# Kernel optimization log

Measured on AMD Instinct MI355X. Metric: run time of the kernel, lower is better.

Reference implementation:

```python
import jax, jax.numpy as jnp
import numpy as np

L1, L2, B, D1, D2, HEADS, M = 1024, 1024, 8, 512, 1024, 16, 1024
DPH = M // HEADS  # 64


def setup_inputs() -> dict:
    key = jax.random.key(0)
    ks = jax.random.split(key, 10)
    w = lambda k, shp: jax.random.normal(k, shp, jnp.float32) * 0.02
    z = lambda n: jnp.zeros((n,), jnp.float32)
    return {
        "ctx_1": jax.random.normal(ks[0], (L1, B, D1), jnp.float32),
        "ctx_2": jax.random.normal(ks[1], (L2, B, D2), jnp.float32),
        "Wk1": w(ks[2], (M, D1)), "bk1": z(M),
        "Wv1": w(ks[3], (M, D1)), "bv1": z(M),
        "Wk2": w(ks[4], (M, D2)), "bk2": z(M),
        "Wv2": w(ks[5], (M, D2)), "bv2": z(M),
        "Wf12": w(ks[6], (M, M)), "bf12": z(M),
        "Wf21": w(ks[7], (M, M)), "bf21": z(M),
    }


def _shape_heads(x):
    # [L, B, M] -> [B, H, L, dph]
    L, Bs, _ = x.shape
    return x.reshape(L, Bs, HEADS, DPH).transpose(1, 2, 0, 3)


def _unshape(x):
    # [B, H, L, dph] -> [L, B, M]
    Bs, Hn, L, d = x.shape
    return x.transpose(2, 0, 1, 3).reshape(L, Bs, Hn * d)


def reference(ctx_1, ctx_2, Wk1, bk1, Wv1, bv1, Wk2, bk2, Wv2, bv2,
              Wf12, bf12, Wf21, bf21):
    k1 = _shape_heads(ctx_1 @ Wk1.T + bk1)  # [B,H,L1,d]
    v1 = _shape_heads(ctx_1 @ Wv1.T + bv1)  # [B,H,L1,d]
    k2 = _shape_heads(ctx_2 @ Wk2.T + bk2)  # [B,H,L2,d]
    v2 = _shape_heads(ctx_2 @ Wv2.T + bv2)  # [B,H,L2,d]

    # scores: key_2 @ key_1^T -> [B, H, L2, L1]
    scores = jnp.einsum('bhqd,bhkd->bhqk', k2, k1)

    # direction 1 -> 2: softmax over dim=2 (the L2 axis), then AV with value_1
    dist_1_to_2 = jax.nn.softmax(scores, axis=2)
    context_1_to_2 = jnp.einsum('bhqk,bhkd->bhqd', dist_1_to_2, v1)  # [B,H,L2,d]
    context_1_to_2 = _unshape(context_1_to_2) @ Wf12.T + bf12        # [L2,B,M]

    # direction 2 -> 1: softmax over dim=1 (the head axis), transpose, AV with value_2
    dist_2_to_1 = jax.nn.softmax(scores, axis=1)
    context_2_to_1 = jnp.einsum('bhqk,bhqd->bhkd', dist_2_to_1, v2)  # [B,H,L1,d]
    context_2_to_1 = _unshape(context_2_to_1) @ Wf21.T + bf21        # [L1,B,M]

    return (context_2_to_1, context_1_to_2)
```

## Files before the change

### kernel.cpp

```cpp
#include <hip/hip_runtime.h>
#include <hip/hip_bf16.h>

constexpr int LQ  = 1024;
constexpr int BN  = 8;
constexpr int D1N = 512;
constexpr int D2N = 1024;
constexpr int HN  = 16;
constexpr int MN  = 1024;
constexpr int DPH = 64;

typedef __attribute__((ext_vector_type(8)))  short bf16x8;
typedef __attribute__((ext_vector_type(2)))  float f32x2;
typedef __attribute__((ext_vector_type(4)))  float f32x4;
typedef __attribute__((ext_vector_type(16))) float f32x16;

__device__ __forceinline__ unsigned short f2bf(float f) {
  unsigned u = __float_as_uint(f);
  u += 0x7FFFu + ((u >> 16) & 1u);
  return (unsigned short)(u >> 16);
}
__device__ __forceinline__ float bf2f(unsigned short u) {
  return __uint_as_float(((unsigned)u) << 16);
}
__device__ __forceinline__ float rcpf(float x) {
  float r;
  asm("v_rcp_f32 %0, %1" : "=v"(r) : "v"(x));
  return r;
}

__device__ __forceinline__ f32x4 mfma16(bf16x8 a, bf16x8 b, f32x4 c) {
  return __builtin_amdgcn_mfma_f32_16x16x32_bf16(a, b, c, 0, 0, 0);
}
__device__ __forceinline__ f32x16 mfma32(bf16x8 a, bf16x8 b, f32x16 c) {
  return __builtin_amdgcn_mfma_f32_32x32x16_bf16(a, b, c, 0, 0, 0);
}
__device__ __forceinline__ f32x16 zero16() {
  f32x16 z;
#pragma unroll
  for (int i = 0; i < 16; ++i) z[i] = 0.f;
  return z;
}

__device__ __forceinline__ unsigned cvtpk(float lo, float hi) {
  unsigned r;
  asm("v_cvt_pk_bf16_f32 %0, %1, %2" : "=v"(r) : "v"(lo), "v"(hi));
  return r;
}

__device__ __forceinline__ void lds_barrier() {
  asm volatile("s_waitcnt lgkmcnt(0)" ::: "memory");
  __builtin_amdgcn_s_barrier();
}

__device__ __forceinline__ bf16x8 pfrag(const float* p) {
  unsigned x0 = cvtpk(p[0], p[1]), y0 = cvtpk(p[4], p[5]);
  unsigned x1 = cvtpk(p[2], p[3]), y1 = cvtpk(p[6], p[7]);
  asm volatile("v_permlane32_swap_b32 %0, %1" : "+v"(x0), "+v"(y0));
  asm volatile("v_permlane32_swap_b32 %0, %1" : "+v"(x1), "+v"(y1));
  union { unsigned u[4]; bf16x8 v; } r;
  r.u[0] = x0; r.u[1] = x1; r.u[2] = y0; r.u[3] = y1;
  return r.v;
}

__device__ __forceinline__ bf16x8 pack8(f32x4 p0, f32x4 p1) {
  bf16x8 o;
  o[0] = (short)f2bf(p0[0]); o[1] = (short)f2bf(p0[1]);
  o[2] = (short)f2bf(p0[2]); o[3] = (short)f2bf(p0[3]);
  o[4] = (short)f2bf(p1[0]); o[5] = (short)f2bf(p1[1]);
  o[6] = (short)f2bf(p1[2]); o[7] = (short)f2bf(p1[3]);
  return o;
}
__device__ __forceinline__ bf16x8 pack8q(f32x4 lo, f32x4 hi) {
  union { unsigned u[4]; bf16x8 v; } r;
  r.u[0] = cvtpk(lo[0], lo[1]); r.u[1] = cvtpk(lo[2], lo[3]);
  r.u[2] = cvtpk(hi[0], hi[1]); r.u[3] = cvtpk(hi[2], hi[3]);
  return r.v;
}

__global__ __launch_bounds__(256) void cvt_kernel(const float* __restrict__ src,
                                                  unsigned short* __restrict__ dst,
                                                  int n8) {
  int i = blockIdx.x * blockDim.x + threadIdx.x;
  if (i >= n8) return;
  const f32x4* s = (const f32x4*)src;
  f32x4 x = s[2 * i], y = s[2 * i + 1];
  ((bf16x8*)dst)[i] = pack8(x, y);
}

template <int K, int MODE, bool AF32>
__device__ __forceinline__ void gemm_body(const void* __restrict__ Ap,
                                          const unsigned short* __restrict__ W,
                                          const float* __restrict__ bias,
                                          void* __restrict__ outp,
                                          int rowb, int colb) {
  __shared__ unsigned short As[128 * 40], Bs[128 * 40];
  const int tid = threadIdx.x, wave = tid >> 6, lane = tid & 63;
  const int lg = lane >> 4, lm = lane & 15;
  const int wrow = (wave >> 1) * 64, wcol = (wave & 1) * 64;
  const int sr = tid >> 1, sh = (tid & 1) * 16;
  const unsigned short* Arow = AF32 ? nullptr
      : (const unsigned short*)Ap + (size_t)(rowb + sr) * K + sh;
  const float* ArowF = AF32 ? (const float*)Ap + (size_t)(rowb + sr) * K + sh
                            : nullptr;
  const unsigned short* Wrow = W + (size_t)(colb + sr) * K + sh;

  f32x4 acc[4][4];
#pragma unroll
  for (int i = 0; i < 4; ++i)
#pragma unroll
    for (int j = 0; j < 4; ++j) acc[i][j] = (f32x4){0.f, 0.f, 0.f, 0.f};

  f32x4 fa0, fa1, fa2, fa3;
  bf16x8 a0, a1, b0, b1;
  if (AF32) {
    fa0 = *(const f32x4*)(ArowF);     fa1 = *(const f32x4*)(ArowF + 4);
    fa2 = *(const f32x4*)(ArowF + 8); fa3 = *(const f32x4*)(ArowF + 12);
  } else {
    a0 = *(const bf16x8*)(Arow);
    a1 = *(const bf16x8*)(Arow + 8);
  }
  b0 = *(const bf16x8*)(Wrow);
  b1 = *(const bf16x8*)(Wrow + 8);

  for (int kk = 0; kk < K; kk += 32) {
    lds_barrier();
    if (AF32) {
      *(bf16x8*)&As[sr * 40 + sh]     = pack8q(fa0, fa1);
      *(bf16x8*)&As[sr * 40 + sh + 8] = pack8q(fa2, fa3);
    } else {
      *(bf16x8*)&As[sr * 40 + sh] = a0;
      *(bf16x8*)&As[sr * 40 + sh + 8] = a1;
    }
    *(bf16x8*)&Bs[sr * 40 + sh] = b0;
    *(bf16x8*)&Bs[sr * 40 + sh + 8] = b1;
    const int kn = (kk + 32 < K) ? kk + 32 : 0;
    if (AF32) {
      fa0 = *(const f32x4*)(ArowF + kn);     fa1 = *(const f32x4*)(ArowF + kn + 4);
      fa2 = *(const f32x4*)(ArowF + kn + 8); fa3 = *(const f32x4*)(ArowF + kn + 12);
    } else {
      a0 = *(const bf16x8*)(Arow + kn);
      a1 = *(const bf16x8*)(Arow + kn + 8);
    }
    b0 = *(const bf16x8*)(Wrow + kn);
    b1 = *(const bf16x8*)(Wrow + kn + 8);
    lds_barrier();
    bf16x8 af[4], wf[4];
#pragma unroll
    for (int i = 0; i < 4; ++i) af[i] = *(const bf16x8*)&As[(wrow + i * 16 + lm) * 40 + lg * 8];
#pragma unroll
    for (int j = 0; j < 4; ++j) wf[j] = *(const bf16x8*)&Bs[(wcol + j * 16 + lm) * 40 + lg * 8];
#pragma unroll
    for (int i = 0; i < 4; ++i)
#pragma unroll
      for (int j = 0; j < 4; ++j) acc[i][j] = mfma16(af[i], wf[j], acc[i][j]);
  }

#pragma unroll
  for (int j = 0; j < 4; ++j) {
    int col = colb + wcol + j * 16 + lm;
    float bs = bias[col];
#pragma unroll
    for (int i = 0; i < 4; ++i) {
#pragma unroll
      for (int r = 0; r < 4; ++r) {
        int row = rowb + wrow + i * 16 + lg * 4 + r;
        float v = acc[i][j][r] + bs;
        if (MODE == 0) {
          int l = row >> 3, bb = row & 7, h = col >> 6, d = col & 63;
          ((unsigned short*)outp)[(((size_t)(bb * HN + h)) * LQ + l) * DPH + d] = f2bf(v);
        } else {
          ((float*)outp)[(size_t)row * MN + col] = v;
        }
      }
    }
  }
}

template <int K>
__global__ __launch_bounds__(256) void gemm_pair_f32_kernel(
    const float* __restrict__ A,
    const unsigned short* __restrict__ W0, const unsigned short* __restrict__ W1,
    const float* __restrict__ b0, const float* __restrict__ b1,
    void* __restrict__ o0, void* __restrict__ o1) {
  const int sel = blockIdx.x & 1;
  gemm_body<K, 0, true>(A, sel ? W1 : W0, sel ? b1 : b0, sel ? o1 : o0,
                        (blockIdx.x >> 1) * 128, blockIdx.y * 128);
}

template <int K>
__global__ __launch_bounds__(256) void gemm_dual_kernel(
    const unsigned short* __restrict__ A0, const unsigned short* __restrict__ A1,
    const unsigned short* __restrict__ W0, const unsigned short* __restrict__ W1,
    const float* __restrict__ b0, const float* __restrict__ b1,
    void* __restrict__ o0, void* __restrict__ o1) {
  const int sel = blockIdx.y >> 3;
  gemm_body<K, 2, false>(sel ? A1 : A0, sel ? W1 : W0, sel ? b1 : b0,
                         sel ? o1 : o0, blockIdx.x * 128, (blockIdx.y & 7) * 128);
}

__global__ __launch_bounds__(256) void transpose_kernel(const unsigned short* __restrict__ V,
                                                        unsigned short* __restrict__ VT,
                                                        const float* __restrict__ scale) {
  __shared__ unsigned short t[64][72];
  int bh = blockIdx.y, l0 = blockIdx.x * 64;
  int tid = threadIdx.x;
  int r = tid >> 2, c0 = (tid & 3) * 16;
  const unsigned short* src = V + ((size_t)bh * LQ + l0 + r) * DPH + c0;
  bf16x8 v0 = *(const bf16x8*)(src);
  bf16x8 v1 = *(const bf16x8*)(src + 8);
  if (scale) {
    float sc = scale[(size_t)bh * LQ + l0 + r];
#pragma unroll
    for (int j = 0; j < 8; ++j) {
      v0[j] = (short)f2bf(bf2f((unsigned short)v0[j]) * sc);
      v1[j] = (short)f2bf(bf2f((unsigned short)v1[j]) * sc);
    }
  }
  *(bf16x8*)&t[r][c0] = v0;
  *(bf16x8*)&t[r][c0 + 8] = v1;
  __syncthreads();
  int d = tid >> 2, lc = (tid & 3) * 16;
  bf16x8 o0, o1;
#pragma unroll
  for (int j = 0; j < 8; ++j) {
    o0[j] = (short)t[lc + j][d];
    o1[j] = (short)t[lc + 8 + j][d];
  }
  unsigned short* dst = VT + ((size_t)bh * DPH + d) * LQ + l0 + lc;
  *(bf16x8*)dst = o0;
  *(bf16x8*)(dst + 8) = o1;
}

__global__ __launch_bounds__(256) void col_reduce_kernel(const unsigned short* __restrict__ K1p,
                                                         const unsigned short* __restrict__ K2p,
                                                         float* __restrict__ inv_colsum) {
  int bh = blockIdx.y, kb = blockIdx.x * 128;
  int wave = threadIdx.x >> 6, lane = threadIdx.x & 63, l31 = lane & 31, sg = lane >> 5;
  int k0w = kb + wave * 32;
  const unsigned short* k1 = K1p + (size_t)bh * LQ * DPH;
  const unsigned short* k2 = K2p + (size_t)bh * LQ * DPH;
  bf16x8 bk[4];
#pragma unroll
  for (int i = 0; i < 4; ++i)
    bk[i] = *(const bf16x8*)(k1 + (size_t)(k0w + l31) * DPH + i * 16 + sg * 8);
  float tot = 0.f;
  for (int q0 = 0; q0 < LQ; q0 += 32) {
    bf16x8 aq[4];
#pragma unroll
    for (int i = 0; i < 4; ++i)
      aq[i] = *(const bf16x8*)(k2 + (size_t)(q0 + l31) * DPH + i * 16 + sg * 8);
    f32x16 cs = zero16();
#pragma unroll
    for (int i = 0; i < 4; ++i) cs = mfma32(aq[i], bk[i], cs);
#pragma unroll
    for (int r = 0; r < 16; ++r) tot += __expf(cs[r]);
  }
  tot += __shfl_xor(tot, 32);
  if (lane < 32) inv_colsum[(size_t)bh * LQ + k0w + lane] = 1.0f / tot;
}

__global__ __launch_bounds__(256) void ctx12_kernel(const unsigned short* __restrict__ K1p,
                                                    const unsigned short* __restrict__ K2p,
                                                    const unsigned short* __restrict__ V1Ts,
                                                    unsigned short* __restrict__ c12) {
  int bh = blockIdx.y, b = bh >> 4, h = bh & 15;
  int wave = threadIdx.x >> 6, lane = threadIdx.x & 63, l31 = lane & 31, sg = lane >> 5;
  int q0 = blockIdx.x * 128 + wave * 32;
  const unsigned short* k1 = K1p + (size_t)bh * LQ * DPH;
  const unsigned short* k2 = K2p + (size_t)bh * LQ * DPH;
  const unsigned short* vt = V1Ts + (size_t)bh * DPH * LQ;

  bf16x8 bq[4];
#pragma unroll
  for (int i = 0; i < 4; ++i)
    bq[i] = *(const bf16x8*)(k2 + (size_t)(q0 + l31) * DPH + i * 16 + sg * 8);

  f32x16 acc0 = zero16(), acc1 = zero16();
  for (int k0 = 0; k0 < LQ; k0 += 32) {
    bf16x8 ak[4];
#pragma unroll
    for (int i = 0; i < 4; ++i)
      ak[i] = *(const bf16x8*)(k1 + (size_t)(k0 + l31) * DPH + i * 16 + sg * 8);
    f32x16 cs = zero16();
#pragma unroll
    for (int i = 0; i < 4; ++i) cs = mfma32(ak[i], bq[i], cs);
    float p[16];
#pragma unroll
    for (int r = 0; r < 16; ++r) p[r] = __expf(cs[r]);
    bf16x8 pa0 = pfrag(p), pa1 = pfrag(p + 8);
    bf16x8 v00 = *(const bf16x8*)(vt + (size_t)l31 * LQ + k0 + sg * 8);
    bf16x8 v01 = *(const bf16x8*)(vt + (size_t)l31 * LQ + k0 + 16 + sg * 8);
    bf16x8 v10 = *(const bf16x8*)(vt + (size_t)(32 + l31) * LQ + k0 + sg * 8);
    bf16x8 v11 = *(const bf16x8*)(vt + (size_t)(32 + l31) * LQ + k0 + 16 + sg * 8);
    acc0 = mfma32(pa0, v00, acc0);
    acc0 = mfma32(pa1, v01, acc0);
    acc1 = mfma32(pa0, v10, acc1);
    acc1 = mfma32(pa1, v11, acc1);
  }
#pragma unroll
  for (int r = 0; r < 16; ++r) {
    int q = q0 + (r & 3) + 8 * (r >> 2) + 4 * sg;
    size_t base = ((size_t)q * BN + b) * MN + h * 64;
    c12[base + l31] = f2bf(acc0[r]);
    c12[base + 32 + l31] = f2bf(acc1[r]);
  }
}

__global__ __launch_bounds__(1024) void ctx21_fused_kernel(const unsigned short* __restrict__ K1p,
                                                           const unsigned short* __restrict__ K2p,
                                                           const unsigned short* __restrict__ V2T,
                                                           unsigned short* __restrict__ c21) {
  constexpr int SP = 66;
  constexpr int WS = 32 * SP;
  __shared__ float strip[16 * WS];
  __shared__ float tot[WS];
  const int b = blockIdx.x, kb = blockIdx.y;
  const int tid = threadIdx.x, wave = tid >> 6, lane = tid & 63;
  const int l31 = lane & 31, sg = lane >> 5;
  const int h = wave, bh = b * HN + h;
  const int k0 = kb * 32;
  const unsigned short* k1 = K1p + (size_t)bh * LQ * DPH;
  const unsigned short* k2 = K2p + (size_t)bh * LQ * DPH;
  const unsigned short* vt = V2T + (size_t)bh * DPH * LQ;
  float* mystrip = &strip[wave * WS];

  const int boff = (tid >> 5) * SP + 2 * (tid & 31);

  bf16x8 bk[4];
#pragma unroll
  for (int i = 0; i < 4; ++i)
    bk[i] = *(const bf16x8*)(k1 + (size_t)(k0 + l31) * DPH + i * 16 + sg * 8);

  f32x16 acc0 = zero16(), acc1 = zero16();

  for (int t = 0; t < LQ / 64; ++t) {
    const int q0 = t * 64;
    bf16x8 v00 = *(const bf16x8*)(vt + (size_t)l31 * LQ + q0 + sg * 8);
    bf16x8 v01 = *(const bf16x8*)(vt + (size_t)l31 * LQ + q0 + 16 + sg * 8);
    bf16x8 v10 = *(const bf16x8*)(vt + (size_t)(32 + l31) * LQ + q0 + sg * 8);
    bf16x8 v11 = *(const bf16x8*)(vt + (size_t)(32 + l31) * LQ + q0 + 16 + sg * 8);
    {
      bf16x8 aqlo[4], aqhi[4];
#pragma unroll
      for (int i = 0; i < 4; ++i) {
        aqlo[i] = *(const bf16x8*)(k2 + (size_t)(q0 + l31) * DPH + i * 16 + sg * 8);
        aqhi[i] = *(const bf16x8*)(k2 + (size_t)(q0 + 32 + l31) * DPH + i * 16 + sg * 8);
      }
      f32x16 cs = zero16();
#pragma unroll
      for (int i = 0; i < 4; ++i) cs = mfma32(aqlo[i], bk[i], cs);
#pragma unroll
      for (int g = 0; g < 4; ++g) {
        int qb = g * 8 + 4 * sg;
        *(f32x2*)&mystrip[l31 * SP + qb]     = (f32x2){__expf(cs[4 * g]),     __expf(cs[4 * g + 1])};
        *(f32x2*)&mystrip[l31 * SP + qb + 2] = (f32x2){__expf(cs[4 * g + 2]), __expf(cs[4 * g + 3])};
      }
      f32x16 cs2 = zero16();
#pragma unroll
      for (int i = 0; i < 4; ++i) cs2 = mfma32(aqhi[i], bk[i], cs2);
#pragma unroll
      for (int g = 0; g < 4; ++g) {
        int qb = 32 + g * 8 + 4 * sg;
        *(f32x2*)&mystrip[l31 * SP + qb]     = (f32x2){__expf(cs2[4 * g]),     __expf(cs2[4 * g + 1])};
        *(f32x2*)&mystrip[l31 * SP + qb + 2] = (f32x2){__expf(cs2[4 * g + 2]), __expf(cs2[4 * g + 3])};
      }
    }
    lds_barrier();
    bf16x8 v20 = *(const bf16x8*)(vt + (size_t)l31 * LQ + q0 + 32 + sg * 8);
    bf16x8 v21 = *(const bf16x8*)(vt + (size_t)l31 * LQ + q0 + 48 + sg * 8);
    bf16x8 v30 = *(const bf16x8*)(vt + (size_t)(32 + l31) * LQ + q0 + 32 + sg * 8);
    bf16x8 v31 = *(const bf16x8*)(vt + (size_t)(32 + l31) * LQ + q0 + 48 + sg * 8);
    {
      f32x2 s = *(const f32x2*)&strip[boff];
#pragma unroll
      for (int w = 1; w < 16; ++w) {
        f32x2 v = *(const f32x2*)&strip[w * WS + boff];
        s.x += v.x; s.y += v.y;
      }
      f32x2 rc; rc.x = rcpf(s.x); rc.y = rcpf(s.y);
      *(f32x2*)&tot[boff] = rc;
    }
    lds_barrier();
    {
      float p8a[8], p8b[8];
#pragma unroll
      for (int g = 0; g < 4; ++g) {
        int qb = g * 8 + 4 * sg;
        f32x2 e0 = *(const f32x2*)&mystrip[l31 * SP + qb];
        f32x2 e1 = *(const f32x2*)&mystrip[l31 * SP + qb + 2];
        f32x2 i0 = *(const f32x2*)&tot[l31 * SP + qb];
        f32x2 i1 = *(const f32x2*)&tot[l31 * SP + qb + 2];
        float* dstp = (g < 2) ? &p8a[(g & 1) * 4] : &p8b[(g & 1) * 4];
        dstp[0] = e0.x * i0.x; dstp[1] = e0.y * i0.y;
        dstp[2] = e1.x * i1.x; dstp[3] = e1.y * i1.y;
      }
      bf16x8 pa0 = pfrag(p8a), pa1 = pfrag(p8b);
      acc0 = mfma32(pa0, v00, acc0);
      acc0 = mfma32(pa1, v01, acc0);
      acc1 = mfma32(pa0, v10, acc1);
      acc1 = mfma32(pa1, v11, acc1);
    }
    {
      float p8c[8], p8d[8];
#pragma unroll
      for (int g = 0; g < 4; ++g) {
        int qb = 32 + g * 8 + 4 * sg;
        f32x2 e0 = *(const f32x2*)&mystrip[l31 * SP + qb];
        f32x2 e1 = *(const f32x2*)&mystrip[l31 * SP + qb + 2];
        f32x2 i0 = *(const f32x2*)&tot[l31 * SP + qb];
        f32x2 i1 = *(const f32x2*)&tot[l31 * SP + qb + 2];
        float* dstp = (g < 2) ? &p8c[(g & 1) * 4] : &p8d[(g & 1) * 4];
        dstp[0] = e0.x * i0.x; dstp[1] = e0.y * i0.y;
        dstp[2] = e1.x * i1.x; dstp[3] = e1.y * i1.y;
      }
      bf16x8 pa2 = pfrag(p8c), pa3 = pfrag(p8d);
      acc0 = mfma32(pa2, v20, acc0);
      acc0 = mfma32(pa3, v21, acc0);
      acc1 = mfma32(pa2, v30, acc1);
      acc1 = mfma32(pa3, v31, acc1);
    }
  }
#pragma unroll
  for (int r = 0; r < 16; ++r) {
    int k = k0 + (r & 3) + 8 * (r >> 2) + 4 * sg;
    size_t base = ((size_t)k * BN + b) * MN + h * 64;
    c21[base + l31] = f2bf(acc0[r]);
    c21[base + 32 + l31] = f2bf(acc1[r]);
  }
}

extern "C" void kernel_launch(void* const* d_in, const int* in_sizes, int n_in,
                              void* d_out, int out_size, void* d_ws, size_t ws_size,
                              hipStream_t stream) {
  const float* ctx1 = (const float*)d_in[0];
  const float* ctx2 = (const float*)d_in[1];
  const float* Wk1 = (const float*)d_in[2];  const float* bk1 = (const float*)d_in[3];
  const float* Wv1 = (const float*)d_in[4];  const float* bv1 = (const float*)d_in[5];
  const float* Wk2 = (const float*)d_in[6];  const float* bk2 = (const float*)d_in[7];
  const float* Wv2 = (const float*)d_in[8];  const float* bv2 = (const float*)d_in[9];
  const float* Wf12 = (const float*)d_in[10]; const float* bf12 = (const float*)d_in[11];
  const float* Wf21 = (const float*)d_in[12]; const float* bf21 = (const float*)d_in[13];

  char* ws = (char*)d_ws;
  size_t off = 0;
  auto alloc = [&](size_t bytes) {
    void* p = ws + off;
    off += (bytes + 255) & ~(size_t)255;
    return p;
  };
  const size_t KV_BYTES = (size_t)BN * HN * LQ * DPH * 2;

  unsigned short* wk1b = (unsigned short*)alloc((size_t)MN * D1N * 2);
  unsigned short* wv1b = (unsigned short*)alloc((size_t)MN * D1N * 2);
  unsigned short* wk2b = (unsigned short*)alloc((size_t)MN * D2N * 2);
  unsigned short* wv2b = (unsigned short*)alloc((size_t)MN * D2N * 2);
  unsigned short* wf12b = (unsigned short*)alloc((size_t)MN * MN * 2);
  unsigned short* wf21b = (unsigned short*)alloc((size_t)MN * MN * 2);
  unsigned short* K1buf = (unsigned short*)alloc(KV_BYTES);
  unsigned short* K2buf = (unsigned short*)alloc(KV_BYTES);
  unsigned short* V1T = (unsigned short*)alloc(KV_BYTES);
  unsigned short* V2T = (unsigned short*)alloc(KV_BYTES);
  float* invcs = (float*)alloc((size_t)BN * HN * LQ * 4);
  unsigned short* c12 = (unsigned short*)alloc(KV_BYTES);
  unsigned short* c21 = (unsigned short*)alloc(KV_BYTES);
  unsigned short* V1tmp = c12;
  unsigned short* V2tmp = c21;

  auto cvt = [&](const float* s, unsigned short* d, int n) {
    int n8 = n / 8;
    cvt_kernel<<<(n8 + 255) / 256, 256, 0, stream>>>(s, d, n8);
  };
  cvt(Wk1, wk1b, MN * D1N);
  cvt(Wv1, wv1b, MN * D1N);
  cvt(Wk2, wk2b, MN * D2N);
  cvt(Wv2, wv2b, MN * D2N);
  cvt(Wf12, wf12b, MN * MN);
  cvt(Wf21, wf21b, MN * MN);

  gemm_pair_f32_kernel<D1N><<<dim3(128, 8), 256, 0, stream>>>(
      ctx1, wk1b, wv1b, bk1, bv1, K1buf, V1tmp);
  gemm_pair_f32_kernel<D2N><<<dim3(128, 8), 256, 0, stream>>>(
      ctx2, wk2b, wv2b, bk2, bv2, K2buf, V2tmp);

  col_reduce_kernel<<<dim3(LQ / 128, BN * HN), 256, 0, stream>>>(K1buf, K2buf, invcs);
  dim3 gt(LQ / 64, BN * HN);
  transpose_kernel<<<gt, 256, 0, stream>>>(V1tmp, V1T, invcs);
  transpose_kernel<<<gt, 256, 0, stream>>>(V2tmp, V2T, nullptr);

  ctx12_kernel<<<dim3(LQ / 128, BN * HN), 256, 0, stream>>>(K1buf, K2buf, V1T, c12);
  ctx21_fused_kernel<<<dim3(BN, LQ / 32), 1024, 0, stream>>>(K1buf, K2buf, V2T, c21);

  float* out0 = (float*)d_out;
  float* out1 = out0 + (size_t)LQ * BN * MN;
  gemm_dual_kernel<MN><<<dim3(64, 16), 256, 0, stream>>>(
      c21, c12, wf21b, wf12b, bf21, bf12, out0, out1);
}
```

Measured before the change: 486.4 us.

## Split ctx21 over query halves with fp32 partials and add-convert pass

Splits the head-softmax AV kernel into two query halves via a third grid dimension, writing fp32 partial context, then sums and converts to bf16 in a new elementwise kernel. Processes 32 queries per iteration with a smaller LDS strip, keeps exp values in registers and prefetches the next K2 tile. Aims to raise block count/occupancy but adds a large fp32 partial write/read and more barriers per query.

```diff
diff --git a/kernel.cpp b/kernel.cpp
--- a/kernel.cpp
+++ b/kernel.cpp
@@ -85,6 +85,19 @@
   const f32x4* s = (const f32x4*)src;
   f32x4 x = s[2 * i], y = s[2 * i + 1];
   ((bf16x8*)dst)[i] = pack8(x, y);
+}
+
+__global__ __launch_bounds__(256) void addcvt_kernel(const float* __restrict__ p0,
+                                                     const float* __restrict__ p1,
+                                                     unsigned short* __restrict__ dst,
+                                                     int n8) {
+  int i = blockIdx.x * blockDim.x + threadIdx.x;
+  if (i >= n8) return;
+  f32x4 a0 = ((const f32x4*)p0)[2 * i],     a1 = ((const f32x4*)p0)[2 * i + 1];
+  f32x4 b0 = ((const f32x4*)p1)[2 * i],     b1 = ((const f32x4*)p1)[2 * i + 1];
+#pragma unroll
+  for (int j = 0; j < 4; ++j) { a0[j] += b0[j]; a1[j] += b1[j]; }
+  ((bf16x8*)dst)[i] = pack8q(a0, a1);
 }
 
 template <int K, int MODE, bool AF32>
@@ -306,15 +319,15 @@
   }
 }
 
-__global__ __launch_bounds__(1024) void ctx21_fused_kernel(const unsigned short* __restrict__ K1p,
-                                                           const unsigned short* __restrict__ K2p,
-                                                           const unsigned short* __restrict__ V2T,
-                                                           unsigned short* __restrict__ c21) {
-  constexpr int SP = 66;
+__global__ __launch_bounds__(1024) void ctx21_part_kernel(const unsigned short* __restrict__ K1p,
+                                                          const unsigned short* __restrict__ K2p,
+                                                          const unsigned short* __restrict__ V2T,
+                                                          float* __restrict__ part) {
+  constexpr int SP = 34;
   constexpr int WS = 32 * SP;
   __shared__ float strip[16 * WS];
   __shared__ float tot[WS];
-  const int b = blockIdx.x, kb = blockIdx.y;
+  const int b = blockIdx.x, kb = blockIdx.y, qh = blockIdx.z;
   const int tid = threadIdx.x, wave = tid >> 6, lane = tid & 63;
   const int l31 = lane & 31, sg = lane >> 5;
   const int h = wave, bh = b * HN + h;
@@ -324,108 +337,81 @@
   const unsigned short* vt = V2T + (size_t)bh * DPH * LQ;
   float* mystrip = &strip[wave * WS];
 
-  const int boff = (tid >> 5) * SP + 2 * (tid & 31);
+  const int bk_ = tid & 31, bq2 = (tid >> 5) * 2;
+  const int tbeg = qh * 16, tend = tbeg + 16;
 
   bf16x8 bk[4];
 #pragma unroll
   for (int i = 0; i < 4; ++i)
     bk[i] = *(const bf16x8*)(k1 + (size_t)(k0 + l31) * DPH + i * 16 + sg * 8);
 
+  bf16x8 aq[4];
+#pragma unroll
+  for (int i = 0; i < 4; ++i)
+    aq[i] = *(const bf16x8*)(k2 + (size_t)(tbeg * 32 + l31) * DPH + i * 16 + sg * 8);
+
   f32x16 acc0 = zero16(), acc1 = zero16();
 
-  for (int t = 0; t < LQ / 64; ++t) {
-    const int q0 = t * 64;
+  for (int t = tbeg; t < tend; ++t) {
+    const int q0 = t * 32;
+    f32x16 cs = zero16();
+#pragma unroll
+    for (int i = 0; i < 4; ++i) cs = mfma32(aq[i], bk[i], cs);
+    const int qn = ((t + 1) & 31) * 32;
+#pragma unroll
+    for (int i = 0; i < 4; ++i)
+      aq[i] = *(const bf16x8*)(k2 + (size_t)(qn + l31) * DPH + i * 16 + sg * 8);
+    float pex[16];
+#pragma unroll
+    for (int r = 0; r < 16; ++r) pex[r] = __expf(cs[r]);
+#pragma unroll
+    for (int g = 0; g < 4; ++g) {
+      int qb = g * 8 + 4 * sg;
+      *(f32x2*)&mystrip[l31 * SP + qb]     = (f32x2){pex[4 * g],     pex[4 * g + 1]};
+      *(f32x2*)&mystrip[l31 * SP + qb + 2] = (f32x2){pex[4 * g + 2], pex[4 * g + 3]};
+    }
     bf16x8 v00 = *(const bf16x8*)(vt + (size_t)l31 * LQ + q0 + sg * 8);
     bf16x8 v01 = *(const bf16x8*)(vt + (size_t)l31 * LQ + q0 + 16 + sg * 8);
     bf16x8 v10 = *(const bf16x8*)(vt + (size_t)(32 + l31) * LQ + q0 + sg * 8);
     bf16x8 v11 = *(const bf16x8*)(vt + (size_t)(32 + l31) * LQ + q0 + 16 + sg * 8);
-    {
-      bf16x8 aqlo[4], aqhi[4];
-#pragma unroll
-      for (int i = 0; i < 4; ++i) {
-        aqlo[i] = *(const bf16x8*)(k2 + (size_t)(q0 + l31) * DPH + i * 16 + sg * 8);
-        aqhi[i] = *(const bf16x8*)(k2 + (size_t)(q0 + 32 + l31) * DPH + i * 16 + sg * 8);
-      }
-      f32x16 cs = zero16();
-#pragma unroll
-      for (int i = 0; i < 4; ++i) cs = mfma32(aqlo[i], bk[i], cs);
-#pragma unroll
-      for (int g = 0; g < 4; ++g) {
-        int qb = g * 8 + 4 * sg;
-        *(f32x2*)&mystrip[l31 * SP + qb]     = (f32x2){__expf(cs[4 * g]),     __expf(cs[4 * g + 1])};
-        *(f32x2*)&mystrip[l31 * SP + qb + 2] = (f32x2){__expf(cs[4 * g + 2]), __expf(cs[4 * g + 3])};
-      }
-      f32x16 cs2 = zero16();
-#pragma unroll
-      for (int i = 0; i < 4; ++i) cs2 = mfma32(aqhi[i], bk[i], cs2);
-#pragma unroll
-      for (int g = 0; g < 4; ++g) {
-        int qb = 32 + g * 8 + 4 * sg;
-        *(f32x2*)&mystrip[l31 * SP + qb]     = (f32x2){__expf(cs2[4 * g]),     __expf(cs2[4 * g + 1])};
-        *(f32x2*)&mystrip[l31 * SP + qb + 2] = (f32x2){__expf(cs2[4 * g + 2]), __expf(cs2[4 * g + 3])};
-      }
-    }
     lds_barrier();
-    bf16x8 v20 = *(const bf16x8*)(vt + (size_t)l31 * LQ + q0 + 32 + sg * 8);
-    bf16x8 v21 = *(const bf16x8*)(vt + (size_t)l31 * LQ + q0 + 48 + sg * 8);
-    bf16x8 v30 = *(const bf16x8*)(vt + (size_t)(32 + l31) * LQ + q0 + 32 + sg * 8);
-    bf16x8 v31 = *(const bf16x8*)(vt + (size_t)(32 + l31) * LQ + q0 + 48 + sg * 8);
-    {
-      f32x2 s = *(const f32x2*)&strip[boff];
+    if (tid < 512) {
+      int off = bk_ * SP + bq2;
+      f32x2 s = *(const f32x2*)&strip[off];
 #pragma unroll
       for (int w = 1; w < 16; ++w) {
-        f32x2 v = *(const f32x2*)&strip[w * WS + boff];
+        f32x2 v = *(const f32x2*)&strip[w * WS + off];
         s.x += v.x; s.y += v.y;
       }
       f32x2 rc; rc.x = rcpf(s.x); rc.y = rcpf(s.y);
-      *(f32x2*)&tot[boff] = rc;
+      *(f32x2*)&tot[off] = rc;
     }
     lds_barrier();
-    {
-      float p8a[8], p8b[8];
-#pragma unroll
-      for (int g = 0; g < 4; ++g) {
-        int qb = g * 8 + 4 * sg;
-        f32x2 e0 = *(const f32x2*)&mystrip[l31 * SP + qb];
-        f32x2 e1 = *(const f32x2*)&mystrip[l31 * SP + qb + 2];
-        f32x2 i0 = *(const f32x2*)&tot[l31 * SP + qb];
-        f32x2 i1 = *(const f32x2*)&tot[l31 * SP + qb + 2];
-        float* dstp = (g < 2) ? &p8a[(g & 1) * 4] : &p8b[(g & 1) * 4];
-        dstp[0] = e0.x * i0.x; dstp[1] = e0.y * i0.y;
-        dstp[2] = e1.x * i1.x; dstp[3] = e1.y * i1.y;
-      }
-      bf16x8 pa0 = pfrag(p8a), pa1 = pfrag(p8b);
-      acc0 = mfma32(pa0, v00, acc0);
-      acc0 = mfma32(pa1, v01, acc0);
-      acc1 = mfma32(pa0, v10, acc1);
-      acc1 = mfma32(pa1, v11, acc1);
-    }
-    {
-      float p8c[8], p8d[8];
-#pragma unroll
-      for (int g = 0; g < 4; ++g) {
-        int qb = 32 + g * 8 + 4 * sg;
-        f32x2 e0 = *(const f32x2*)&mystrip[l31 * SP + qb];
-        f32x2 e1 = *(const f32x2*)&mystrip[l31 * SP + qb + 2];
-        f32x2 i0 = *(const f32x2*)&tot[l31 * SP + qb];
-        f32x2 i1 = *(const f32x2*)&tot[l31 * SP + qb + 2];
-        float* dstp = (g < 2) ? &p8c[(g & 1) * 4] : &p8d[(g & 1) * 4];
-        dstp[0] = e0.x * i0.x; dstp[1] = e0.y * i0.y;
-        dstp[2] = e1.x * i1.x; dstp[3] = e1.y * i1.y;
-      }
-      bf16x8 pa2 = pfrag(p8c), pa3 = pfrag(p8d);
-      acc0 = mfma32(pa2, v20, acc0);
-      acc0 = mfma32(pa3, v21, acc0);
-      acc1 = mfma32(pa2, v30, acc1);
-      acc1 = mfma32(pa3, v31, acc1);
-    }
-  }
+    float p8a[8], p8b[8];
+#pragma unroll
+    for (int g = 0; g < 4; ++g) {
+      int qb = g * 8 + 4 * sg;
+      f32x2 t0 = *(const f32x2*)&tot[l31 * SP + qb];
+      f32x2 t1 = *(const f32x2*)&tot[l31 * SP + qb + 2];
+      float* dstp = (g < 2) ? &p8a[(g & 1) * 4] : &p8b[(g & 1) * 4];
+      dstp[0] = pex[4 * g]     * t0.x;
+      dstp[1] = pex[4 * g + 1] * t0.y;
+      dstp[2] = pex[4 * g + 2] * t1.x;
+      dstp[3] = pex[4 * g + 3] * t1.y;
+    }
+    bf16x8 pa0 = pfrag(p8a), pa1 = pfrag(p8b);
+    acc0 = mfma32(pa0, v00, acc0);
+    acc0 = mfma32(pa1, v01, acc0);
+    acc1 = mfma32(pa0, v10, acc1);
+    acc1 = mfma32(pa1, v11, acc1);
+  }
+  float* dst = part + (size_t)qh * (8192 * (size_t)MN);
 #pragma unroll
   for (int r = 0; r < 16; ++r) {
     int k = k0 + (r & 3) + 8 * (r >> 2) + 4 * sg;
     size_t base = ((size_t)k * BN + b) * MN + h * 64;
-    c21[base + l31] = f2bf(acc0[r]);
-    c21[base + 32 + l31] = f2bf(acc1[r]);
+    dst[base + l31] = acc0[r];
+    dst[base + 32 + l31] = acc1[r];
   }
 }
 
@@ -463,6 +449,7 @@
   float* invcs = (float*)alloc((size_t)BN * HN * LQ * 4);
   unsigned short* c12 = (unsigned short*)alloc(KV_BYTES);
   unsigned short* c21 = (unsigned short*)alloc(KV_BYTES);
+  float* c21p = (float*)alloc((size_t)2 * 8192 * MN * 4);
   unsigned short* V1tmp = c12;
   unsigned short* V2tmp = c21;
 
@@ -488,7 +475,9 @@
   transpose_kernel<<<gt, 256, 0, stream>>>(V2tmp, V2T, nullptr);
 
   ctx12_kernel<<<dim3(LQ / 128, BN * HN), 256, 0, stream>>>(K1buf, K2buf, V1T, c12);
-  ctx21_fused_kernel<<<dim3(BN, LQ / 32), 1024, 0, stream>>>(K1buf, K2buf, V2T, c21);
+  ctx21_part_kernel<<<dim3(BN, LQ / 32, 2), 1024, 0, stream>>>(K1buf, K2buf, V2T, c21p);
+  addcvt_kernel<<<(8192 * MN / 8 + 255) / 256, 256, 0, stream>>>(
+      c21p, c21p + (size_t)8192 * MN, c21, 8192 * MN / 8);
 
   float* out0 = (float*)d_out;
   float* out1 = out0 + (size_t)LQ * BN * MN;
```

Result: slower. 518.3 us (+6.6%).
